# Kernel optimization log

Hardware: AMD Instinct MI355X
Metric: run time of the kernel (lower is better)

The kernel has to match this reference:

```python
import jax, jax.numpy as jnp
import numpy as np

NUM_ATOMS = 4_000_000
NUM_TYPES = 11

def setup_inputs() -> dict:
    key = jax.random.key(0)
    k1, k2 = jax.random.split(key)
    input_coords = jax.random.normal(k1, (3 * NUM_ATOMS,), dtype=jnp.float32)
    atom_types = jax.random.randint(k2, (NUM_ATOMS,), 0, NUM_TYPES, dtype=jnp.int64)
    return {"input_coords": input_coords, "atom_types": atom_types, "num_atom_types": NUM_TYPES}

def reference(input_coords, atom_types, num_atom_types):
    # counts per atom type  [T]
    counts = jnp.bincount(atom_types, length=num_atom_types).astype(jnp.int32)
    # exclusive prefix sum -> bucket offsets  [T]
    offsets = (jnp.cumsum(counts) - counts).astype(jnp.int32)
    # stable sort by type reproduces the C++ bucket fill order:
    # atoms of the same type keep their original relative order.
    perm = jnp.argsort(atom_types, stable=True)  # [N] source index for each output slot
    coords3 = input_coords.reshape(-1, 3)        # [N,3]
    typed_coords = coords3[perm].reshape(-1)     # [3N] type-grouped flat coords
    return typed_coords, counts, offsets
```

## Files before the change

### kernel.cpp

```cpp
#include <hip/hip_runtime.h>

#define NTYPES 11
#define BLOCK  256
#define ITEMS  8
#define CHUNK  (BLOCK * ITEMS)
#define MAXCH  32

__global__ __launch_bounds__(BLOCK) void hist_kernel(
    const int* __restrict__ types, int N, int B, int* __restrict__ bc,
    unsigned int* __restrict__ packed) {
  __shared__ int shCnt[NTYPES];
  const int tid = threadIdx.x;
  const int b = blockIdx.x;
  if (tid < NTYPES) shCnt[tid] = 0;
  __syncthreads();

  const int run = b * CHUNK + tid * ITEMS;
  int cnt[NTYPES];
#pragma unroll
  for (int t = 0; t < NTYPES; ++t) cnt[t] = 0;

  if (run < N) {
    const int4* p = (const int4*)(types + run);
    int4 a0 = p[0], a1 = p[1];
    int ty[ITEMS] = {a0.x, a0.y, a0.z, a0.w, a1.x, a1.y, a1.z, a1.w};
    unsigned int pk = 0;
#pragma unroll
    for (int k = 0; k < ITEMS; ++k) pk |= ((unsigned int)ty[k]) << (4 * k);
    packed[b * BLOCK + tid] = pk;
#pragma unroll
    for (int k = 0; k < ITEMS; ++k) {
#pragma unroll
      for (int t = 0; t < NTYPES; ++t) cnt[t] += (ty[k] == t) ? 1 : 0;
    }
  }

  const int lane = tid & 63;
#pragma unroll
  for (int t = 0; t < NTYPES; ++t) {
    int v = cnt[t];
    for (int o = 32; o >= 1; o >>= 1) v += __shfl_down(v, o);
    if (lane == 0) atomicAdd(&shCnt[t], v);
  }
  __syncthreads();
  if (tid < NTYPES) bc[tid * B + b] = shCnt[tid];
}

__global__ __launch_bounds__(NTYPES * 64) void scan_kernel(
    const int* __restrict__ bc, int B, int* __restrict__ scanOut,
    int* __restrict__ offs, float* __restrict__ outTail) {
  __shared__ int totals[NTYPES];
  const int lane = threadIdx.x & 63;
  const int t = threadIdx.x >> 6;
  const int nch = (B + 63) >> 6;

  int x[MAXCH];
#pragma unroll
  for (int c = 0; c < MAXCH; ++c) {
    const int idx = c * 64 + lane;
    x[c] = (c < nch && idx < B) ? bc[t * B + idx] : 0;
  }

  int carry = 0;
#pragma unroll
  for (int c = 0; c < MAXCH; ++c) {
    if (c >= nch) break;
    int incl = x[c];
#pragma unroll
    for (int o = 1; o < 64; o <<= 1) {
      int v = __shfl_up(incl, o);
      if (lane >= o) incl += v;
    }
    incl += carry;
    const int idx = c * 64 + lane;
    if (idx < B) scanOut[t * B + idx] = incl - x[c];
    carry = __shfl(incl, 63);
  }
  if (lane == 0) totals[t] = carry;
  __syncthreads();

  if (threadIdx.x == 0) {
    int off = 0;
    for (int u = 0; u < NTYPES; ++u) {
      const int c = totals[u];
      offs[u] = off;
      outTail[u] = (float)c;
      outTail[NTYPES + u] = (float)off;
      off += c;
    }
  }
}

__global__ __launch_bounds__(BLOCK) void scatter_kernel(
    const float* __restrict__ coords, const unsigned int* __restrict__ packed,
    const int* __restrict__ scanOut, const int* __restrict__ offs, int N,
    int B, float* __restrict__ out) {
  __shared__ float shC[CHUNK * 3];
  __shared__ int wtot[NTYPES][4];
  __shared__ int shOff[NTYPES + 1];
  __shared__ int shDelta[NTYPES];

  const int tid = threadIdx.x;
  const int b = blockIdx.x;
  const int lane = tid & 63;
  const int wave = tid >> 6;
  const int run = b * CHUNK + tid * ITEMS;
  const bool active = (run < N);

  int ty[ITEMS];
  int cnt[NTYPES];
#pragma unroll
  for (int t = 0; t < NTYPES; ++t) cnt[t] = 0;
#pragma unroll
  for (int k = 0; k < ITEMS; ++k) ty[k] = -1;

  float c[ITEMS * 3];
  if (active) {
    const unsigned int pk = packed[b * BLOCK + tid];
#pragma unroll
    for (int k = 0; k < ITEMS; ++k) ty[k] = (int)((pk >> (4 * k)) & 0xFu);
    const float4* cp = (const float4*)(coords + (size_t)run * 3);
#pragma unroll
    for (int q = 0; q < (ITEMS * 3) / 4; ++q) {
      float4 v = cp[q];
      c[4 * q + 0] = v.x;
      c[4 * q + 1] = v.y;
      c[4 * q + 2] = v.z;
      c[4 * q + 3] = v.w;
    }
#pragma unroll
    for (int k = 0; k < ITEMS; ++k) {
#pragma unroll
      for (int t = 0; t < NTYPES; ++t) cnt[t] += (ty[k] == t) ? 1 : 0;
    }
  }

  int rank[NTYPES];
#pragma unroll
  for (int t = 0; t < NTYPES; ++t) {
    int incl = cnt[t];
#pragma unroll
    for (int o = 1; o < 64; o <<= 1) {
      int v = __shfl_up(incl, o);
      if (lane >= o) incl += v;
    }
    if (lane == 63) wtot[t][wave] = incl;
    rank[t] = incl - cnt[t];
  }
  __syncthreads();

  if (tid < NTYPES) {
    int loc = 0;
    for (int u = 0; u < tid; ++u)
      loc += wtot[u][0] + wtot[u][1] + wtot[u][2] + wtot[u][3];
    shOff[tid] = loc;
    shDelta[tid] = 3 * (offs[tid] + scanOut[tid * B + b] - loc);
    if (tid == NTYPES - 1) {
      shOff[NTYPES] =
          loc + wtot[tid][0] + wtot[tid][1] + wtot[tid][2] + wtot[tid][3];
    }
  }
  __syncthreads();

#pragma unroll
  for (int t = 0; t < NTYPES; ++t) {
    int wb = 0;
#pragma unroll
    for (int w = 0; w < 3; ++w) wb += (w < wave) ? wtot[t][w] : 0;
    rank[t] += wb + shOff[t];
  }

  if (active) {
#pragma unroll
    for (int k = 0; k < ITEMS; ++k) {
      const int t0 = ty[k];
      int slot = 0;
#pragma unroll
      for (int t = 0; t < NTYPES; ++t) {
        if (t0 == t) {
          slot = rank[t];
          rank[t] += 1;
        }
      }
      shC[3 * slot + 0] = c[3 * k + 0];
      shC[3 * slot + 1] = c[3 * k + 1];
      shC[3 * slot + 2] = c[3 * k + 2];
    }
  }
  __syncthreads();

  const int total3 = 3 * shOff[NTYPES];
  int offr3[NTYPES];
  int dlt[NTYPES];
#pragma unroll
  for (int t = 0; t < NTYPES; ++t) {
    offr3[t] = 3 * shOff[t];
    dlt[t] = shDelta[t];
  }
  const float4* shC4 = (const float4*)shC;
#pragma unroll
  for (int k = 0; k < (ITEMS * 3) / 4; ++k) {
    const int w = k * BLOCK + tid;
    const int j0 = 4 * w;
    if (j0 < total3) {
      const float4 v = shC4[w];
      int d0 = dlt[0], d3 = dlt[0];
#pragma unroll
      for (int t = 1; t < NTYPES; ++t) {
        d0 = (j0 >= offr3[t]) ? dlt[t] : d0;
        d3 = (j0 + 3 >= offr3[t]) ? dlt[t] : d3;
      }
      if (d0 == d3) {
        out[j0 + d0 + 0] = v.x;
        out[j0 + d0 + 1] = v.y;
        out[j0 + d0 + 2] = v.z;
        out[j0 + d0 + 3] = v.w;
      } else {
        int d1 = dlt[0], d2 = dlt[0];
#pragma unroll
        for (int t = 1; t < NTYPES; ++t) {
          d1 = (j0 + 1 >= offr3[t]) ? dlt[t] : d1;
          d2 = (j0 + 2 >= offr3[t]) ? dlt[t] : d2;
        }
        out[j0 + d0 + 0] = v.x;
        out[j0 + d1 + 1] = v.y;
        out[j0 + d2 + 2] = v.z;
        out[j0 + d3 + 3] = v.w;
      }
    }
  }
}

extern "C" void kernel_launch(void* const* d_in, const int* in_sizes, int n_in,
                              void* d_out, int out_size, void* d_ws,
                              size_t ws_size, hipStream_t stream) {
  const float* coords = (const float*)d_in[0];
  const int* types = (const int*)d_in[1];
  const int N = in_sizes[1];
  const int B = (N + CHUNK - 1) / CHUNK;

  int* bc = (int*)d_ws;
  int* scanOut = bc + NTYPES * B;
  int* offs = scanOut + NTYPES * B;
  unsigned int* packed = (unsigned int*)(offs + NTYPES + 1);
  float* out = (float*)d_out;
  float* outTail = out + (size_t)3 * N;

  hist_kernel<<<B, BLOCK, 0, stream>>>(types, N, B, bc, packed);
  scan_kernel<<<1, NTYPES * 64, 0, stream>>>(bc, B, scanOut, offs, outTail);
  scatter_kernel<<<B, BLOCK, 0, stream>>>(coords, packed, scanOut, offs, N, B,
                                          out);
}
```

Measured before the change: 137.3 us.

## Compute per-block local slot ranks in histogram kernel and pass 16-bit slots

The in-block stable ranking (wave-level prefix scans over types, cross-wave offsets) moves from the scatter kernel into the histogram kernel. The histogram kernel now writes a 16-bit local slot per atom instead of 4-bit packed types. The scatter kernel only reads those slots, loads coordinates and stages them in shared memory, so it drops one barrier and a large block of shuffle and register work. The cost is four times more intermediate traffic (2 bytes per atom written and read instead of half a byte), plus a short serial global-read loop in the scatter kernel to rebuild block offsets from the bucket counts.

```diff
diff --git a/kernel.cpp b/kernel.cpp
--- a/kernel.cpp
+++ b/kernel.cpp
@@ -8,26 +8,29 @@
 
 __global__ __launch_bounds__(BLOCK) void hist_kernel(
     const int* __restrict__ types, int N, int B, int* __restrict__ bc,
-    unsigned int* __restrict__ packed) {
-  __shared__ int shCnt[NTYPES];
+    unsigned short* __restrict__ slots) {
+  __shared__ int wtot[NTYPES][4];
+  __shared__ int shOff[NTYPES];
   const int tid = threadIdx.x;
   const int b = blockIdx.x;
-  if (tid < NTYPES) shCnt[tid] = 0;
-  __syncthreads();
-
+  const int lane = tid & 63;
+  const int wave = tid >> 6;
   const int run = b * CHUNK + tid * ITEMS;
+  const bool active = (run < N);
+
+  int ty[ITEMS];
   int cnt[NTYPES];
 #pragma unroll
   for (int t = 0; t < NTYPES; ++t) cnt[t] = 0;
-
-  if (run < N) {
+#pragma unroll
+  for (int k = 0; k < ITEMS; ++k) ty[k] = -1;
+
+  if (active) {
     const int4* p = (const int4*)(types + run);
     int4 a0 = p[0], a1 = p[1];
-    int ty[ITEMS] = {a0.x, a0.y, a0.z, a0.w, a1.x, a1.y, a1.z, a1.w};
-    unsigned int pk = 0;
-#pragma unroll
-    for (int k = 0; k < ITEMS; ++k) pk |= ((unsigned int)ty[k]) << (4 * k);
-    packed[b * BLOCK + tid] = pk;
+    int tt[ITEMS] = {a0.x, a0.y, a0.z, a0.w, a1.x, a1.y, a1.z, a1.w};
+#pragma unroll
+    for (int k = 0; k < ITEMS; ++k) ty[k] = tt[k];
 #pragma unroll
     for (int k = 0; k < ITEMS; ++k) {
 #pragma unroll
@@ -35,15 +38,60 @@
     }
   }
 
-  const int lane = tid & 63;
+  int rank[NTYPES];
 #pragma unroll
   for (int t = 0; t < NTYPES; ++t) {
-    int v = cnt[t];
-    for (int o = 32; o >= 1; o >>= 1) v += __shfl_down(v, o);
-    if (lane == 0) atomicAdd(&shCnt[t], v);
-  }
-  __syncthreads();
-  if (tid < NTYPES) bc[tid * B + b] = shCnt[tid];
+    int incl = cnt[t];
+#pragma unroll
+    for (int o = 1; o < 64; o <<= 1) {
+      int v = __shfl_up(incl, o);
+      if (lane >= o) incl += v;
+    }
+    if (lane == 63) wtot[t][wave] = incl;
+    rank[t] = incl - cnt[t];
+  }
+  __syncthreads();
+
+  if (tid < NTYPES) {
+    int loc = 0;
+    for (int u = 0; u < tid; ++u)
+      loc += wtot[u][0] + wtot[u][1] + wtot[u][2] + wtot[u][3];
+    shOff[tid] = loc;
+    bc[tid * B + b] =
+        wtot[tid][0] + wtot[tid][1] + wtot[tid][2] + wtot[tid][3];
+  }
+  __syncthreads();
+
+#pragma unroll
+  for (int t = 0; t < NTYPES; ++t) {
+    int wb = 0;
+#pragma unroll
+    for (int w = 0; w < 3; ++w) wb += (w < wave) ? wtot[t][w] : 0;
+    rank[t] += wb + shOff[t];
+  }
+
+  if (active) {
+    unsigned short sl[ITEMS];
+#pragma unroll
+    for (int k = 0; k < ITEMS; ++k) {
+      const int t0 = ty[k];
+      int slot = 0;
+#pragma unroll
+      for (int t = 0; t < NTYPES; ++t) {
+        if (t0 == t) {
+          slot = rank[t];
+          rank[t] += 1;
+        }
+      }
+      sl[k] = (unsigned short)slot;
+    }
+    int4 sv;
+    sv.x = (int)sl[0] | ((int)sl[1] << 16);
+    sv.y = (int)sl[2] | ((int)sl[3] << 16);
+    sv.z = (int)sl[4] | ((int)sl[5] << 16);
+    sv.w = (int)sl[6] | ((int)sl[7] << 16);
+    *(int4*)(slots + run) = sv;
+  }
 }
 
 __global__ __launch_bounds__(NTYPES * 64) void scan_kernel(
@@ -92,34 +140,34 @@
 }
 
 __global__ __launch_bounds__(BLOCK) void scatter_kernel(
-    const float* __restrict__ coords, const unsigned int* __restrict__ packed,
-    const int* __restrict__ scanOut, const int* __restrict__ offs, int N,
-    int B, float* __restrict__ out) {
+    const float* __restrict__ coords, const unsigned short* __restrict__ slots,
+    const int* __restrict__ bc, const int* __restrict__ scanOut,
+    const int* __restrict__ offs, int N, int B, float* __restrict__ out) {
   __shared__ float shC[CHUNK * 3];
-  __shared__ int wtot[NTYPES][4];
   __shared__ int shOff[NTYPES + 1];
   __shared__ int shDelta[NTYPES];
 
   const int tid = threadIdx.x;
   const int b = blockIdx.x;
-  const int lane = tid & 63;
-  const int wave = tid >> 6;
   const int run = b * CHUNK + tid * ITEMS;
   const bool active = (run < N);
 
-  int ty[ITEMS];
-  int cnt[NTYPES];
-#pragma unroll
-  for (int t = 0; t < NTYPES; ++t) cnt[t] = 0;
-#pragma unroll
-  for (int k = 0; k < ITEMS; ++k) ty[k] = -1;
-
-  float c[ITEMS * 3];
+  if (tid < NTYPES) {
+    int loc = 0;
+    for (int u = 0; u < tid; ++u) loc += bc[u * B + b];
+    shOff[tid] = loc;
+    shDelta[tid] = 3 * (offs[tid] + scanOut[tid * B + b] - loc);
+    if (tid == NTYPES - 1) shOff[NTYPES] = loc + bc[tid * B + b];
+  }
+
   if (active) {
-    const unsigned int pk = packed[b * BLOCK + tid];
-#pragma unroll
-    for (int k = 0; k < ITEMS; ++k) ty[k] = (int)((pk >> (4 * k)) & 0xFu);
+    const int4 sv = *(const int4*)(slots + run);
+    int sl[ITEMS] = {sv.x & 0xFFFF, (sv.x >> 16) & 0xFFFF,
+                     sv.y & 0xFFFF, (sv.y >> 16) & 0xFFFF,
+                     sv.z & 0xFFFF, (sv.z >> 16) & 0xFFFF,
+                     sv.w & 0xFFFF, (sv.w >> 16) & 0xFFFF};
     const float4* cp = (const float4*)(coords + (size_t)run * 3);
+    float c[ITEMS * 3];
 #pragma unroll
     for (int q = 0; q < (ITEMS * 3) / 4; ++q) {
       float4 v = cp[q];
@@ -130,61 +178,10 @@
     }
 #pragma unroll
     for (int k = 0; k < ITEMS; ++k) {
-#pragma unroll
-      for (int t = 0; t < NTYPES; ++t) cnt[t] += (ty[k] == t) ? 1 : 0;
-    }
-  }
-
-  int rank[NTYPES];
-#pragma unroll
-  for (int t = 0; t < NTYPES; ++t) {
-    int incl = cnt[t];
-#pragma unroll
-    for (int o = 1; o < 64; o <<= 1) {
-      int v = __shfl_up(incl, o);
-      if (lane >= o) incl += v;
-    }
-    if (lane == 63) wtot[t][wave] = incl;
-    rank[t] = incl - cnt[t];
-  }
-  __syncthreads();
-
-  if (tid < NTYPES) {
-    int loc = 0;
-    for (int u = 0; u < tid; ++u)
-      loc += wtot[u][0] + wtot[u][1] + wtot[u][2] + wtot[u][3];
-    shOff[tid] = loc;
-    shDelta[tid] = 3 * (offs[tid] + scanOut[tid * B + b] - loc);
-    if (tid == NTYPES - 1) {
-      shOff[NTYPES] =
-          loc + wtot[tid][0] + wtot[tid][1] + wtot[tid][2] + wtot[tid][3];
-    }
-  }
-  __syncthreads();
-
-#pragma unroll
-  for (int t = 0; t < NTYPES; ++t) {
-    int wb = 0;
-#pragma unroll
-    for (int w = 0; w < 3; ++w) wb += (w < wave) ? wtot[t][w] : 0;
-    rank[t] += wb + shOff[t];
-  }
-
-  if (active) {
-#pragma unroll
-    for (int k = 0; k < ITEMS; ++k) {
-      const int t0 = ty[k];
-      int slot = 0;
-#pragma unroll
-      for (int t = 0; t < NTYPES; ++t) {
-        if (t0 == t) {
-          slot = rank[t];
-          rank[t] += 1;
-        }
-      }
-      shC[3 * slot + 0] = c[3 * k + 0];
-      shC[3 * slot + 1] = c[3 * k + 1];
-      shC[3 * slot + 2] = c[3 * k + 2];
+      const int s = sl[k];
+      shC[3 * s + 0] = c[3 * k + 0];
+      shC[3 * s + 1] = c[3 * k + 1];
+      shC[3 * s + 2] = c[3 * k + 2];
     }
   }
   __syncthreads();
@@ -242,12 +239,12 @@
   int* bc = (int*)d_ws;
   int* scanOut = bc + NTYPES * B;
   int* offs = scanOut + NTYPES * B;
-  unsigned int* packed = (unsigned int*)(offs + NTYPES + 1);
+  unsigned short* slots = (unsigned short*)(offs + NTYPES + 1);
   float* out = (float*)d_out;
   float* outTail = out + (size_t)3 * N;
 
-  hist_kernel<<<B, BLOCK, 0, stream>>>(types, N, B, bc, packed);
+  hist_kernel<<<B, BLOCK, 0, stream>>>(types, N, B, bc, slots);
   scan_kernel<<<1, NTYPES * 64, 0, stream>>>(bc, B, scanOut, offs, outTail);
-  scatter_kernel<<<B, BLOCK, 0, stream>>>(coords, packed, scanOut, offs, N, B,
-                                          out);
-}
+  scatter_kernel<<<B, BLOCK, 0, stream>>>(coords, slots, bc, scanOut, offs, N,
+                                          B, out);
+}
```

Result: no change. 138.7 us (+1.1%).
